# Performance work log

Measured on AMD Instinct MI355X. Metric: run time of the kernel, lower is better.

Reference implementation:

```python
import jax, jax.numpy as jnp
import numpy as np

N = 500_000   # total nodes across the batch of session graphs
B = 8192      # number of graphs
D = 128       # input_dim == output_dim (fc_out is None)
H = 128       # hidden_dim


def setup_inputs() -> dict:
    key = jax.random.key(0)
    ks = jax.random.split(key, 7)
    x_invar = jax.random.normal(ks[0], (N, D), jnp.float32)
    x_var = jax.random.normal(ks[1], (N, D), jnp.float32)
    s = 1.0 / np.sqrt(D)
    Wu = jax.random.normal(ks[2], (H, D), jnp.float32) * s
    bu = jnp.zeros((H,), jnp.float32)
    Wv = jax.random.normal(ks[3], (H, D), jnp.float32) * s
    We = jax.random.normal(ks[4], (1, H), jnp.float32) * (1.0 / np.sqrt(H))
    # sorted segment ids; guarantee every graph has >= 1 node
    seg_ids = jnp.sort(jnp.concatenate([
        jnp.arange(B, dtype=jnp.int32),
        jax.random.randint(ks[5], (N - B,), 0, B, dtype=jnp.int32),
    ]))
    # last node index of each graph = cumsum(counts) - 1
    counts = jax.ops.segment_sum(jnp.ones((N,), jnp.int32), seg_ids, num_segments=B)
    last_nodes = (jnp.cumsum(counts) - 1).astype(jnp.int32)
    return dict(x_invar=x_invar, x_var=x_var, Wu=Wu, bu=bu, Wv=Wv, We=We,
                seg_ids=seg_ids, last_nodes=last_nodes, num_graphs=B)


def _segment_softmax(e, seg, num_segments):
    # e: [M]; numerically stable per-segment softmax
    m = jax.ops.segment_max(e, seg, num_segments=num_segments)
    ex = jnp.exp(e - m[seg])
    den = jax.ops.segment_sum(ex, seg, num_segments=num_segments)
    return ex / den[seg]


def reference(x_invar, x_var, Wu, bu, Wv, We, seg_ids, last_nodes, num_graphs):
    # hybrid granularity, order=1: per-graph [invar; var] node rows.
    # Segment softmax/sum are permutation-invariant within a segment, so we
    # concatenate globally and double the segment ids.
    feats = jnp.concatenate([x_invar, x_var], axis=0)          # [2N, D]
    seg2 = jnp.concatenate([seg_ids, seg_ids], axis=0)         # [2N]
    feat_u = feats @ Wu.T + bu                                 # [2N, H]
    v_invar = (x_invar[last_nodes] @ Wv.T)[seg2]               # [2N, H]
    v_var = (x_var[last_nodes] @ Wv.T)[seg2]                   # [2N, H]
    e_invar = (jax.nn.sigmoid(feat_u + v_invar) @ We.T)[:, 0]  # [2N]
    e_var = (jax.nn.sigmoid(feat_u + v_var) @ We.T)[:, 0]      # [2N]
    a_invar = _segment_softmax(e_invar, seg2, num_graphs)[:, None]
    a_var = _segment_softmax(e_var, seg2, num_graphs)[:, None]
    rst_invar = jax.ops.segment_sum(feats * a_invar, seg2, num_segments=num_graphs)  # [B, D]
    rst_var = jax.ops.segment_sum(feats * a_var, seg2, num_segments=num_graphs)      # [B, D]
    return rst_invar[:, None, :], rst_var[:, None, :]          # [B, 1, D] each (order=1)
```

## Files before the change

kernel.cpp:

```cpp
#include <hip/hip_runtime.h>
#include <stdint.h>

typedef short short8 __attribute__((ext_vector_type(8)));
typedef float f32x4 __attribute__((ext_vector_type(4)));

#define D 128
#define LOG2E 1.44269504088896340736f
#define GPB 4

__device__ __forceinline__ unsigned short f2bf(float f) {
    union { float f; unsigned u; } v; v.f = f;
    unsigned u = v.u;
    unsigned r = (u + 0x7FFFu + ((u >> 16) & 1u)) >> 16;
    return (unsigned short)r;
}

__device__ __forceinline__ unsigned packbf(float x, float y) {
    unsigned ux = __float_as_uint(x) + 0x8000u;
    unsigned uy = __float_as_uint(y) + 0x8000u;
    return __builtin_amdgcn_perm(uy, ux, 0x07060302u);
}

template <int C>
__device__ __forceinline__ float dpp_add(float x) {
    int y = __builtin_amdgcn_update_dpp(0, __float_as_int(x), C, 0xF, 0xF, true);
    return x + __int_as_float(y);
}
__device__ __forceinline__ float red16(float x) {
    x = dpp_add<0xB1>(x);
    x = dpp_add<0x4E>(x);
    x = dpp_add<0x141>(x);
    x = dpp_add<0x140>(x);
    return x;
}

__global__ __launch_bounds__(256) void pack_wu(const float* __restrict__ Wu,
                                               short8* __restrict__ frag) {
    int tid = blockIdx.x * 256 + threadIdx.x;
    int nt = tid >> 8, kk = (tid >> 6) & 3, l = tid & 63;
    int col = nt * 16 + (l & 15);
    int kb  = kk * 32 + ((l >> 4) * 8);
    short8 o;
#pragma unroll
    for (int j = 0; j < 8; ++j) o[j] = (short)f2bf(Wu[col * D + kb + j] * LOG2E);
    frag[tid] = o;
}

__global__ __launch_bounds__(256) void gate_k(const float* __restrict__ xI,
                                              const float* __restrict__ xV,
                                              const float* __restrict__ Wv,
                                              const float* __restrict__ bu,
                                              const int* __restrict__ lastn,
                                              float* __restrict__ cIb,
                                              float* __restrict__ cVb, int B) {
    __shared__ __align__(16) float xs[4][2][D];
    int t = threadIdx.x, h = t & 127, st = t >> 7;
    float bias = bu[h];
    const float4* wv4 = (const float4*)(Wv + (size_t)h * D);
    const float* src = st ? xV : xI;
    float* dst = st ? cVb : cIb;
    int g0 = blockIdx.x * 16;
    for (int p = 0; p < 4; ++p) {
        int gb = g0 + p * 4;
#pragma unroll
        for (int j = 0; j < 4; ++j) {
            int gg = gb + j; if (gg >= B) gg = B - 1;
            xs[j][st][h] = src[(size_t)lastn[gg] * D + h];
        }
        __syncthreads();
        const float4* x0 = (const float4*)xs[0][st];
        const float4* x1 = (const float4*)xs[1][st];
        const float4* x2 = (const float4*)xs[2][st];
        const float4* x3 = (const float4*)xs[3][st];
        float a0 = 0.f, a1 = 0.f, a2 = 0.f, a3 = 0.f;
#pragma unroll
        for (int i = 0; i < 32; ++i) {
            float4 w = wv4[i], b;
            b = x0[i]; a0 += w.x*b.x + w.y*b.y + w.z*b.z + w.w*b.w;
            b = x1[i]; a1 += w.x*b.x + w.y*b.y + w.z*b.z + w.w*b.w;
            b = x2[i]; a2 += w.x*b.x + w.y*b.y + w.z*b.z + w.w*b.w;
            b = x3[i]; a3 += w.x*b.x + w.y*b.y + w.z*b.z + w.w*b.w;
        }
        if (gb + 0 < B) dst[(size_t)(gb+0)*D + h] = __builtin_amdgcn_exp2f(-(a0+bias)*LOG2E);
        if (gb + 1 < B) dst[(size_t)(gb+1)*D + h] = __builtin_amdgcn_exp2f(-(a1+bias)*LOG2E);
        if (gb + 2 < B) dst[(size_t)(gb+2)*D + h] = __builtin_amdgcn_exp2f(-(a2+bias)*LOG2E);
        if (gb + 3 < B) dst[(size_t)(gb+3)*D + h] = __builtin_amdgcn_exp2f(-(a3+bias)*LOG2E);
        __syncthreads();
    }
}

__global__ __launch_bounds__(256) void attn_main(
    const float* __restrict__ xI, const float* __restrict__ xV,
    const float* __restrict__ We, const int* __restrict__ lastn,
    const float* __restrict__ cIb, const float* __restrict__ cVb,
    const short8* __restrict__ fragG, float* __restrict__ out, int B) {
    __shared__ short8 bfrag[2048];
    __shared__ __align__(16) float wt[4][16][2];
    __shared__ float cmbA[2][4][D];
    __shared__ float cmbL[2][4];

    int t = threadIdx.x, lane = t & 63, w = t >> 6;

    {
        const uint4* srcf = (const uint4*)fragG;
        uint4* dst = (uint4*)bfrag;
#pragma unroll
        for (int i = 0; i < 8; ++i) dst[i * 256 + t] = srcf[i * 256 + t];
    }
    float WeR[8];
#pragma unroll
    for (int nt = 0; nt < 8; ++nt) WeR[nt] = We[nt * 16 + (lane & 15)] * LOG2E;
    __syncthreads();

    int g0 = blockIdx.x * GPB;
    int sNext = (g0 == 0) ? 0 : (lastn[g0 - 1] + 1);

    for (int gi = 0; gi < GPB; ++gi) {
        int g = g0 + gi;
        int s = sNext;
        int e = lastn[g] + 1;
        sNext = e;
        int n = e - s;

        float cIr[8], cVr[8];
#pragma unroll
        for (int nt = 0; nt < 8; ++nt) {
            int col = nt * 16 + (lane & 15);
            cIr[nt] = cIb[(size_t)g * D + col];
            cVr[nt] = cVb[(size_t)g * D + col];
        }

        float lIs = 0.f, lVs = 0.f;
        float aI0 = 0.f, aI1 = 0.f, aV0 = 0.f, aV1 = 0.f;

        int ch = (n + 15) >> 4;
        int total = 2 * ch;

        float4 pre[8];
        auto issuePre = [&](int cc) {
            int hf = (cc >= ch) ? 1 : 0;
            const float* sp = (hf ? xV : xI) + ((size_t)s << 7);
            int bb = (cc - hf * ch) << 4;
            int ar = bb + (lane & 15); if (ar > n - 1) ar = n - 1;
            const float* rp = sp + ((size_t)ar << 7) + ((lane >> 4) << 3);
#pragma unroll
            for (int kk = 0; kk < 4; ++kk) {
                pre[2 * kk]     = *(const float4*)(rp + kk * 32);
                pre[2 * kk + 1] = *(const float4*)(rp + kk * 32 + 4);
            }
        };

        if (w < total) issuePre(w);

        for (int c = w; c < total; c += 4) {
            int hf = (c >= ch) ? 1 : 0;
            const float* srcs = (hf ? xV : xI) + ((size_t)s << 7);
            int base = (c - hf * ch) << 4;

            short8 af[4];
#pragma unroll
            for (int kk = 0; kk < 4; ++kk) {
                float4 f0 = pre[2 * kk], f1 = pre[2 * kk + 1];
                union { unsigned u[4]; short8 s8; } cv;
                cv.u[0] = packbf(f0.x, f0.y);
                cv.u[1] = packbf(f0.z, f0.w);
                cv.u[2] = packbf(f1.x, f1.y);
                cv.u[3] = packbf(f1.z, f1.w);
                af[kk] = cv.s8;
            }

            if (c + 4 < total) issuePre(c + 4);

            float pI[4] = {0.f, 0.f, 0.f, 0.f}, pV[4] = {0.f, 0.f, 0.f, 0.f};
#pragma unroll
            for (int nt = 0; nt < 8; ++nt) {
                f32x4 dacc = {0.f, 0.f, 0.f, 0.f};
#pragma unroll
                for (int kk = 0; kk < 4; ++kk)
                    dacc = __builtin_amdgcn_mfma_f32_16x16x32_bf16(
                        af[kk], bfrag[nt * 256 + kk * 64 + lane], dacc, 0, 0, 0);
#pragma unroll
                for (int q = 0; q < 4; ++q) {
                    float t2 = __builtin_amdgcn_exp2f(-dacc[q]);
                    float dI = fmaf(t2, cIr[nt], 1.f);
                    float dV = fmaf(t2, cVr[nt], 1.f);
                    float rr = __builtin_amdgcn_rcpf(dI * dV);
                    pI[q] = fmaf(WeR[nt], dV * rr, pI[q]);
                    pV[q] = fmaf(WeR[nt], dI * rr, pV[q]);
                }
            }

            const float2* s2 = (const float2*)srcs;
            float2 fr[16];
#pragma unroll
            for (int r = 0; r < 16; ++r) {
                int rr = base + r; if (rr > n - 1) rr = n - 1;
                fr[r] = s2[((size_t)rr << 6) + lane];
            }

#pragma unroll
            for (int q = 0; q < 4; ++q) { pI[q] = red16(pI[q]); pV[q] = red16(pV[q]); }
            if (base + 16 > n) {
#pragma unroll
                for (int q = 0; q < 4; ++q) {
                    int r = ((lane >> 4) << 2) + q;
                    if (base + r >= n) { pI[q] = -__builtin_inff(); pV[q] = -__builtin_inff(); }
                }
            }
            float wIq[4], wVq[4];
#pragma unroll
            for (int q = 0; q < 4; ++q) {
                wIq[q] = __builtin_amdgcn_exp2f(pI[q]);
                wVq[q] = __builtin_amdgcn_exp2f(pV[q]);
            }
            lIs += (wIq[0] + wIq[1]) + (wIq[2] + wIq[3]);
            lVs += (wVq[0] + wVq[1]) + (wVq[2] + wVq[3]);

            if ((lane & 15) == 0) {
                int gq = lane >> 4;
                float4 w0 = {wIq[0], wVq[0], wIq[1], wVq[1]};
                float4 w1 = {wIq[2], wVq[2], wIq[3], wVq[3]};
                *(float4*)&wt[w][gq * 4 + 0][0] = w0;
                *(float4*)&wt[w][gq * 4 + 2][0] = w1;
            }

#pragma unroll
            for (int r = 0; r < 16; ++r) {
                float2 f = fr[r];
                float2 wv = *(const float2*)&wt[w][r][0];
                aI0 = fmaf(wv.x, f.x, aI0); aI1 = fmaf(wv.x, f.y, aI1);
                aV0 = fmaf(wv.y, f.x, aV0); aV1 = fmaf(wv.y, f.y, aV1);
            }
        }

        lIs += __shfl_xor(lIs, 16); lIs += __shfl_xor(lIs, 32);
        lVs += __shfl_xor(lVs, 16); lVs += __shfl_xor(lVs, 32);

        __syncthreads();
        {
            float2 vI = {aI0, aI1}, vV = {aV0, aV1};
            *(float2*)&cmbA[0][w][lane * 2] = vI;
            *(float2*)&cmbA[1][w][lane * 2] = vV;
        }
        if (lane == 0) { cmbL[0][w] = lIs; cmbL[1][w] = lVs; }
        __syncthreads();
        {
            int st = t >> 7, d = t & 127;
            float Ls = (cmbL[st][0] + cmbL[st][1]) + (cmbL[st][2] + cmbL[st][3]);
            float A  = (cmbA[st][0][d] + cmbA[st][1][d]) +
                       (cmbA[st][2][d] + cmbA[st][3][d]);
            out[(size_t)st * B * D + (size_t)g * D + d] = A * __builtin_amdgcn_rcpf(Ls);
        }
    }
}

extern "C" void kernel_launch(void* const* d_in, const int* in_sizes, int n_in,
                              void* d_out, int out_size, void* d_ws, size_t ws_size,
                              hipStream_t stream) {
    const float* xI    = (const float*)d_in[0];
    const float* xV    = (const float*)d_in[1];
    const float* Wu    = (const float*)d_in[2];
    const float* bu    = (const float*)d_in[3];
    const float* Wv    = (const float*)d_in[4];
    const float* We    = (const float*)d_in[5];
    const int*   lastn = (const int*)d_in[7];
    const int B = in_sizes[7];

    float*  cIb   = (float*)d_ws;
    float*  cVb   = cIb + (size_t)B * D;
    short8* fragW = (short8*)(cVb + (size_t)B * D);

    pack_wu<<<8, 256, 0, stream>>>(Wu, fragW);
    gate_k<<<(B + 15) / 16, 256, 0, stream>>>(xI, xV, Wv, bu, lastn, cIb, cVb, B);
    attn_main<<<B / GPB, 256, 0, stream>>>(xI, xV, We, lastn, cIb, cVb, fragW,
                                           (float*)d_out, B);
}
```

Baseline: 250.4 us.

## Stage node tiles into LDS via global_load_lds and pack three graph groups per block

Node feature tiles are now loaded once per chunk straight into swizzled LDS buffers using the direct global-to-LDS load. Both the bf16 MFMA A-fragments and the per-row float2 aggregation reads come from that staged copy, so the second global read of the same rows goes away. Blocks grow to 768 threads holding three independent 4-wave groups of two graphs each. The bf16 weight fragments in shared memory are therefore amortised over more waves. In exchange, LDS use rises sharply (about 130KB of staging), which limits occupancy, and full vmcnt/lgkmcnt waits serialise the prefetch.

```diff
diff --git a/kernel.cpp b/kernel.cpp
--- a/kernel.cpp
+++ b/kernel.cpp
@@ -6,7 +6,9 @@
 
 #define D 128
 #define LOG2E 1.44269504088896340736f
-#define GPB 4
+#define NGG  2
+#define NGRP 3
+#define GPBLK (NGG * NGRP)
 
 __device__ __forceinline__ unsigned short f2bf(float f) {
     union { float f; unsigned u; } v; v.f = f;
@@ -32,6 +34,12 @@
     x = dpp_add<0x141>(x);
     x = dpp_add<0x140>(x);
     return x;
+}
+
+__device__ __forceinline__ void gld16(const float* g, float* l) {
+    __builtin_amdgcn_global_load_lds(
+        (const __attribute__((address_space(1))) void*)g,
+        (__attribute__((address_space(3))) void*)l, 16, 0, 0);
 }
 
 __global__ __launch_bounds__(256) void pack_wu(const float* __restrict__ Wu,
@@ -89,78 +97,106 @@
     }
 }
 
-__global__ __launch_bounds__(256) void attn_main(
+__global__ __launch_bounds__(768) void attn_main(
     const float* __restrict__ xI, const float* __restrict__ xV,
     const float* __restrict__ We, const int* __restrict__ lastn,
     const float* __restrict__ cIb, const float* __restrict__ cVb,
     const short8* __restrict__ fragG, float* __restrict__ out, int B) {
     __shared__ short8 bfrag[2048];
-    __shared__ __align__(16) float wt[4][16][2];
-    __shared__ float cmbA[2][4][D];
-    __shared__ float cmbL[2][4];
+    __shared__ __align__(16) float stage[12][2048];
+    __shared__ __align__(16) float wt[12][16][2];
+    __shared__ float cmbA[NGRP][2][4][D];
+    __shared__ float cmbL[NGRP][2][4];
 
     int t = threadIdx.x, lane = t & 63, w = t >> 6;
+    int grp = w >> 2, wiw = w & 3;
 
     {
         const uint4* srcf = (const uint4*)fragG;
         uint4* dst = (uint4*)bfrag;
 #pragma unroll
-        for (int i = 0; i < 8; ++i) dst[i * 256 + t] = srcf[i * 256 + t];
+        for (int i = 0; i < 3; ++i) {
+            int idx = i * 768 + t;
+            if (idx < 2048) dst[idx] = srcf[idx];
+        }
     }
     float WeR[8];
 #pragma unroll
     for (int nt = 0; nt < 8; ++nt) WeR[nt] = We[nt * 16 + (lane & 15)] * LOG2E;
     __syncthreads();
 
-    int g0 = blockIdx.x * GPB;
-    int sNext = (g0 == 0) ? 0 : (lastn[g0 - 1] + 1);
-
-    for (int gi = 0; gi < GPB; ++gi) {
+    float* rb = &stage[w][0];
+    const char* rbc = (const char*)rb;
+
+    int loff[8];
+#pragma unroll
+    for (int i = 0; i < 8; ++i) {
+        int row = (i << 1) + (lane >> 5);
+        loff[i] = (row << 7) + (((lane & 31) ^ (row & 7)) << 2);
+    }
+    int arow = lane & 15;
+    int sw = (arow & 7) << 4;
+    int ab0 = ((arow << 9) + ((lane >> 4) << 5)) ^ sw;
+    int ab1 = ((arow << 9) + ((lane >> 4) << 5) + 16) ^ sw;
+
+    int g0 = blockIdx.x * GPBLK + grp * NGG;
+
+    for (int gi = 0; gi < NGG; ++gi) {
         int g = g0 + gi;
-        int s = sNext;
-        int e = lastn[g] + 1;
-        sNext = e;
-        int n = e - s;
-
+        bool act = (g < B);
+        int s = 0, n = 0, ch = 0, total = 0;
         float cIr[8], cVr[8];
-#pragma unroll
-        for (int nt = 0; nt < 8; ++nt) {
-            int col = nt * 16 + (lane & 15);
-            cIr[nt] = cIb[(size_t)g * D + col];
-            cVr[nt] = cVb[(size_t)g * D + col];
+        if (act) {
+            s = (g == 0) ? 0 : (lastn[g - 1] + 1);
+            n = lastn[g] + 1 - s;
+#pragma unroll
+            for (int nt = 0; nt < 8; ++nt) {
+                int col = nt * 16 + (lane & 15);
+                cIr[nt] = cIb[(size_t)g * D + col];
+                cVr[nt] = cVb[(size_t)g * D + col];
+            }
+            ch = (n + 15) >> 4;
+            total = 2 * ch;
         }
 
         float lIs = 0.f, lVs = 0.f;
         float aI0 = 0.f, aI1 = 0.f, aV0 = 0.f, aV1 = 0.f;
 
-        int ch = (n + 15) >> 4;
-        int total = 2 * ch;
-
-        float4 pre[8];
-        auto issuePre = [&](int cc) {
+        auto issue = [&](int cc) {
             int hf = (cc >= ch) ? 1 : 0;
             const float* sp = (hf ? xV : xI) + ((size_t)s << 7);
             int bb = (cc - hf * ch) << 4;
-            int ar = bb + (lane & 15); if (ar > n - 1) ar = n - 1;
-            const float* rp = sp + ((size_t)ar << 7) + ((lane >> 4) << 3);
+            if (bb + 16 <= n) {
+                const float* pb = sp + ((size_t)bb << 7);
+#pragma unroll
+                for (int i = 0; i < 8; ++i)
+                    gld16(pb + loff[i], rb + (i << 8) + (lane << 2));
+            } else {
+#pragma unroll
+                for (int i = 0; i < 8; ++i) {
+                    int row = (i << 1) + (lane >> 5);
+                    int rr = bb + row; if (rr > n - 1) rr = n - 1;
+                    int lu = (lane & 31) ^ (row & 7);
+                    gld16(sp + ((size_t)rr << 7) + (lu << 2),
+                          rb + (i << 8) + (lane << 2));
+                }
+            }
+        };
+
+        if (wiw < total) issue(wiw);
+
+        for (int c = wiw; c < total; c += 4) {
+            int hf = (c >= ch) ? 1 : 0;
+            int base = (c - hf * ch) << 4;
+
+            asm volatile("s_waitcnt vmcnt(0)" ::: "memory");
+            __builtin_amdgcn_sched_barrier(0);
+
+            short8 af[4];
 #pragma unroll
             for (int kk = 0; kk < 4; ++kk) {
-                pre[2 * kk]     = *(const float4*)(rp + kk * 32);
-                pre[2 * kk + 1] = *(const float4*)(rp + kk * 32 + 4);
-            }
-        };
-
-        if (w < total) issuePre(w);
-
-        for (int c = w; c < total; c += 4) {
-            int hf = (c >= ch) ? 1 : 0;
-            const float* srcs = (hf ? xV : xI) + ((size_t)s << 7);
-            int base = (c - hf * ch) << 4;
-
-            short8 af[4];
-#pragma unroll
-            for (int kk = 0; kk < 4; ++kk) {
-                float4 f0 = pre[2 * kk], f1 = pre[2 * kk + 1];
+                float4 f0 = *(const float4*)(rbc + ab0 + (kk << 7));
+                float4 f1 = *(const float4*)(rbc + ab1 + (kk << 7));
                 union { unsigned u[4]; short8 s8; } cv;
                 cv.u[0] = packbf(f0.x, f0.y);
                 cv.u[1] = packbf(f0.z, f0.w);
@@ -168,8 +204,14 @@
                 cv.u[3] = packbf(f1.z, f1.w);
                 af[kk] = cv.s8;
             }
-
-            if (c + 4 < total) issuePre(c + 4);
+            float2 fr[16];
+#pragma unroll
+            for (int r = 0; r < 16; ++r)
+                fr[r] = *(const float2*)(rbc + ((((r << 9) + (lane << 3)))
+                                               ^ ((r & 7) << 4)));
+            asm volatile("s_waitcnt lgkmcnt(0)" ::: "memory");
+            __builtin_amdgcn_sched_barrier(0);
+            if (c + 4 < total) issue(c + 4);
 
             float pI[4] = {0.f, 0.f, 0.f, 0.f}, pV[4] = {0.f, 0.f, 0.f, 0.f};
 #pragma unroll
@@ -189,15 +231,6 @@
                     pV[q] = fmaf(WeR[nt], dI * rr, pV[q]);
                 }
             }
-
-            const float2* s2 = (const float2*)srcs;
-            float2 fr[16];
-#pragma unroll
-            for (int r = 0; r < 16; ++r) {
-                int rr = base + r; if (rr > n - 1) rr = n - 1;
-                fr[r] = s2[((size_t)rr << 6) + lane];
-            }
-
 #pragma unroll
             for (int q = 0; q < 4; ++q) { pI[q] = red16(pI[q]); pV[q] = red16(pV[q]); }
             if (base + 16 > n) {
@@ -237,18 +270,20 @@
         lVs += __shfl_xor(lVs, 16); lVs += __shfl_xor(lVs, 32);
 
         __syncthreads();
-        {
+        if (act) {
             float2 vI = {aI0, aI1}, vV = {aV0, aV1};
-            *(float2*)&cmbA[0][w][lane * 2] = vI;
-            *(float2*)&cmbA[1][w][lane * 2] = vV;
-        }
-        if (lane == 0) { cmbL[0][w] = lIs; cmbL[1][w] = lVs; }
+            *(float2*)&cmbA[grp][0][wiw][lane * 2] = vI;
+            *(float2*)&cmbA[grp][1][wiw][lane * 2] = vV;
+            if (lane == 0) { cmbL[grp][0][wiw] = lIs; cmbL[grp][1][wiw] = lVs; }
+        }
         __syncthreads();
-        {
-            int st = t >> 7, d = t & 127;
-            float Ls = (cmbL[st][0] + cmbL[st][1]) + (cmbL[st][2] + cmbL[st][3]);
-            float A  = (cmbA[st][0][d] + cmbA[st][1][d]) +
-                       (cmbA[st][2][d] + cmbA[st][3][d]);
+        if (act) {
+            int tig = wiw * 64 + lane;
+            int st = tig >> 7, d = tig & 127;
+            float Ls = (cmbL[grp][st][0] + cmbL[grp][st][1]) +
+                       (cmbL[grp][st][2] + cmbL[grp][st][3]);
+            float A  = (cmbA[grp][st][0][d] + cmbA[grp][st][1][d]) +
+                       (cmbA[grp][st][2][d] + cmbA[grp][st][3][d]);
             out[(size_t)st * B * D + (size_t)g * D + d] = A * __builtin_amdgcn_rcpf(Ls);
         }
     }
@@ -272,6 +307,7 @@
 
     pack_wu<<<8, 256, 0, stream>>>(Wu, fragW);
     gate_k<<<(B + 15) / 16, 256, 0, stream>>>(xI, xV, Wv, bu, lastn, cIb, cVb, B);
-    attn_main<<<B / GPB, 256, 0, stream>>>(xI, xV, We, lastn, cIb, cVb, fragW,
-                                           (float*)d_out, B);
-}
+    int nblk = (B + GPBLK - 1) / GPBLK;
+    attn_main<<<nblk, 768, 0, stream>>>(xI, xV, We, lastn, cIb, cVb, fragW,
+                                        (float*)d_out, B);
+}
```

After: 701.1 us. 180% more time.

## Tile attention over fixed node rows with atomic segment accumulation

Applied to the files above, without the earlier changes.

Replaces the per-graph block loop (4 graphs per block, variable work) with fixed 256-row tiles over the flat node array per stream. Gate values are gathered per row via seg ids, and partial weighted sums and softmax denominators are flushed with global atomics at segment boundaries. A final kernel then normalizes. This targets load imbalance from variable graph sizes, at the cost of atomics, memsets, an extra launch, per-row seg loads, and loss of the register prefetch pipeline. Softmax still has no max subtraction, as before.

```diff
diff --git a/kernel.cpp b/kernel.cpp
--- a/kernel.cpp
+++ b/kernel.cpp
@@ -6,7 +6,6 @@
 
 #define D 128
 #define LOG2E 1.44269504088896340736f
-#define GPB 4
 
 __device__ __forceinline__ unsigned short f2bf(float f) {
     union { float f; unsigned u; } v; v.f = f;
@@ -89,18 +88,18 @@
     }
 }
 
-__global__ __launch_bounds__(256) void attn_main(
+__global__ __launch_bounds__(256) void tile_k(
     const float* __restrict__ xI, const float* __restrict__ xV,
-    const float* __restrict__ We, const int* __restrict__ lastn,
+    const float* __restrict__ We, const int* __restrict__ seg,
     const float* __restrict__ cIb, const float* __restrict__ cVb,
-    const short8* __restrict__ fragG, float* __restrict__ out, int B) {
+    const short8* __restrict__ fragG,
+    float* __restrict__ acc,
+    float* __restrict__ lAcc,
+    int N, int B, int nBS) {
     __shared__ short8 bfrag[2048];
     __shared__ __align__(16) float wt[4][16][2];
-    __shared__ float cmbA[2][4][D];
-    __shared__ float cmbL[2][4];
 
     int t = threadIdx.x, lane = t & 63, w = t >> 6;
-
     {
         const uint4* srcf = (const uint4*)fragG;
         uint4* dst = (uint4*)bfrag;
@@ -112,146 +111,132 @@
     for (int nt = 0; nt < 8; ++nt) WeR[nt] = We[nt * 16 + (lane & 15)] * LOG2E;
     __syncthreads();
 
-    int g0 = blockIdx.x * GPB;
-    int sNext = (g0 == 0) ? 0 : (lastn[g0 - 1] + 1);
-
-    for (int gi = 0; gi < GPB; ++gi) {
-        int g = g0 + gi;
-        int s = sNext;
-        int e = lastn[g] + 1;
-        sNext = e;
-        int n = e - s;
-
-        float cIr[8], cVr[8];
+    int bid = blockIdx.x;
+    int strm = (bid >= nBS) ? 1 : 0;
+    const float* xs = strm ? xV : xI;
+    float* accI = acc;
+    float* accV = acc + (size_t)B * D;
+    int rowBase = (bid - strm * nBS) * 256 + w * 64;
+
+    int curG = -1;
+    float sI0=0.f, sI1=0.f, sV0=0.f, sV1=0.f, lsI=0.f, lsV=0.f;
+
+    for (int rg = 0; rg < 4; ++rg) {
+        int rbase = rowBase + rg * 16;
+        if (rbase >= N) break;
+
+        int arow = rbase + (lane & 15); if (arow > N - 1) arow = N - 1;
+        const float* rp = xs + (size_t)arow * D + ((lane >> 4) << 3);
+        short8 af[4];
+#pragma unroll
+        for (int kk = 0; kk < 4; ++kk) {
+            float4 f0 = *(const float4*)(rp + kk * 32);
+            float4 f1 = *(const float4*)(rp + kk * 32 + 4);
+            union { unsigned u[4]; short8 s8; } cv;
+            cv.u[0] = packbf(f0.x, f0.y);
+            cv.u[1] = packbf(f0.z, f0.w);
+            cv.u[2] = packbf(f1.x, f1.y);
+            cv.u[3] = packbf(f1.z, f1.w);
+            af[kk] = cv.s8;
+        }
+
+        int g4D[4];
+#pragma unroll
+        for (int q = 0; q < 4; ++q) {
+            int r = rbase + ((lane >> 4) << 2) + q; if (r > N - 1) r = N - 1;
+            g4D[q] = seg[r] << 7;
+        }
+
+        float pI[4] = {0.f,0.f,0.f,0.f}, pV[4] = {0.f,0.f,0.f,0.f};
 #pragma unroll
         for (int nt = 0; nt < 8; ++nt) {
             int col = nt * 16 + (lane & 15);
-            cIr[nt] = cIb[(size_t)g * D + col];
-            cVr[nt] = cVb[(size_t)g * D + col];
-        }
-
-        float lIs = 0.f, lVs = 0.f;
-        float aI0 = 0.f, aI1 = 0.f, aV0 = 0.f, aV1 = 0.f;
-
-        int ch = (n + 15) >> 4;
-        int total = 2 * ch;
-
-        float4 pre[8];
-        auto issuePre = [&](int cc) {
-            int hf = (cc >= ch) ? 1 : 0;
-            const float* sp = (hf ? xV : xI) + ((size_t)s << 7);
-            int bb = (cc - hf * ch) << 4;
-            int ar = bb + (lane & 15); if (ar > n - 1) ar = n - 1;
-            const float* rp = sp + ((size_t)ar << 7) + ((lane >> 4) << 3);
-#pragma unroll
-            for (int kk = 0; kk < 4; ++kk) {
-                pre[2 * kk]     = *(const float4*)(rp + kk * 32);
-                pre[2 * kk + 1] = *(const float4*)(rp + kk * 32 + 4);
-            }
-        };
-
-        if (w < total) issuePre(w);
-
-        for (int c = w; c < total; c += 4) {
-            int hf = (c >= ch) ? 1 : 0;
-            const float* srcs = (hf ? xV : xI) + ((size_t)s << 7);
-            int base = (c - hf * ch) << 4;
-
-            short8 af[4];
-#pragma unroll
-            for (int kk = 0; kk < 4; ++kk) {
-                float4 f0 = pre[2 * kk], f1 = pre[2 * kk + 1];
-                union { unsigned u[4]; short8 s8; } cv;
-                cv.u[0] = packbf(f0.x, f0.y);
-                cv.u[1] = packbf(f0.z, f0.w);
-                cv.u[2] = packbf(f1.x, f1.y);
-                cv.u[3] = packbf(f1.z, f1.w);
-                af[kk] = cv.s8;
-            }
-
-            if (c + 4 < total) issuePre(c + 4);
-
-            float pI[4] = {0.f, 0.f, 0.f, 0.f}, pV[4] = {0.f, 0.f, 0.f, 0.f};
-#pragma unroll
-            for (int nt = 0; nt < 8; ++nt) {
-                f32x4 dacc = {0.f, 0.f, 0.f, 0.f};
-#pragma unroll
-                for (int kk = 0; kk < 4; ++kk)
-                    dacc = __builtin_amdgcn_mfma_f32_16x16x32_bf16(
-                        af[kk], bfrag[nt * 256 + kk * 64 + lane], dacc, 0, 0, 0);
-#pragma unroll
-                for (int q = 0; q < 4; ++q) {
-                    float t2 = __builtin_amdgcn_exp2f(-dacc[q]);
-                    float dI = fmaf(t2, cIr[nt], 1.f);
-                    float dV = fmaf(t2, cVr[nt], 1.f);
-                    float rr = __builtin_amdgcn_rcpf(dI * dV);
-                    pI[q] = fmaf(WeR[nt], dV * rr, pI[q]);
-                    pV[q] = fmaf(WeR[nt], dI * rr, pV[q]);
+            float cI4[4], cV4[4];
+#pragma unroll
+            for (int q = 0; q < 4; ++q) {
+                cI4[q] = cIb[g4D[q] + col];
+                cV4[q] = cVb[g4D[q] + col];
+            }
+            f32x4 dacc = {0.f, 0.f, 0.f, 0.f};
+#pragma unroll
+            for (int kk = 0; kk < 4; ++kk)
+                dacc = __builtin_amdgcn_mfma_f32_16x16x32_bf16(
+                    af[kk], bfrag[nt * 256 + kk * 64 + lane], dacc, 0, 0, 0);
+#pragma unroll
+            for (int q = 0; q < 4; ++q) {
+                float t2 = __builtin_amdgcn_exp2f(-dacc[q]);
+                float dI = fmaf(t2, cI4[q], 1.f);
+                float dV = fmaf(t2, cV4[q], 1.f);
+                float rr = __builtin_amdgcn_rcpf(dI * dV);
+                pI[q] = fmaf(WeR[nt], dV * rr, pI[q]);
+                pV[q] = fmaf(WeR[nt], dI * rr, pV[q]);
+            }
+        }
+#pragma unroll
+        for (int q = 0; q < 4; ++q) { pI[q] = red16(pI[q]); pV[q] = red16(pV[q]); }
+        if (rbase + 16 > N) {
+#pragma unroll
+            for (int q = 0; q < 4; ++q) {
+                int r = rbase + ((lane >> 4) << 2) + q;
+                if (r >= N) { pI[q] = -__builtin_inff(); pV[q] = -__builtin_inff(); }
+            }
+        }
+        float wIq[4], wVq[4];
+#pragma unroll
+        for (int q = 0; q < 4; ++q) {
+            wIq[q] = __builtin_amdgcn_exp2f(pI[q]);
+            wVq[q] = __builtin_amdgcn_exp2f(pV[q]);
+        }
+        if ((lane & 15) == 0) {
+            int gq = lane >> 4;
+            float4 w0 = {wIq[0], wVq[0], wIq[1], wVq[1]};
+            float4 w1 = {wIq[2], wVq[2], wIq[3], wVq[3]};
+            *(float4*)&wt[w][gq * 4 + 0][0] = w0;
+            *(float4*)&wt[w][gq * 4 + 2][0] = w1;
+        }
+
+        const float2* s2 = (const float2*)xs;
+        for (int r = 0; r < 16; ++r) {
+            int rr = rbase + r; int rc = rr > N - 1 ? N - 1 : rr;
+            int gr = seg[rc];
+            if (gr != curG) {
+                if (curG >= 0) {
+                    size_t o = ((size_t)curG << 7) + (lane << 1);
+                    atomicAdd(&accI[o], sI0);     atomicAdd(&accI[o + 1], sI1);
+                    atomicAdd(&accV[o], sV0);     atomicAdd(&accV[o + 1], sV1);
+                    if (lane == 0) {
+                        atomicAdd(&lAcc[curG], lsI);
+                        atomicAdd(&lAcc[B + curG], lsV);
+                    }
                 }
-            }
-
-            const float2* s2 = (const float2*)srcs;
-            float2 fr[16];
-#pragma unroll
-            for (int r = 0; r < 16; ++r) {
-                int rr = base + r; if (rr > n - 1) rr = n - 1;
-                fr[r] = s2[((size_t)rr << 6) + lane];
-            }
-
-#pragma unroll
-            for (int q = 0; q < 4; ++q) { pI[q] = red16(pI[q]); pV[q] = red16(pV[q]); }
-            if (base + 16 > n) {
-#pragma unroll
-                for (int q = 0; q < 4; ++q) {
-                    int r = ((lane >> 4) << 2) + q;
-                    if (base + r >= n) { pI[q] = -__builtin_inff(); pV[q] = -__builtin_inff(); }
-                }
-            }
-            float wIq[4], wVq[4];
-#pragma unroll
-            for (int q = 0; q < 4; ++q) {
-                wIq[q] = __builtin_amdgcn_exp2f(pI[q]);
-                wVq[q] = __builtin_amdgcn_exp2f(pV[q]);
-            }
-            lIs += (wIq[0] + wIq[1]) + (wIq[2] + wIq[3]);
-            lVs += (wVq[0] + wVq[1]) + (wVq[2] + wVq[3]);
-
-            if ((lane & 15) == 0) {
-                int gq = lane >> 4;
-                float4 w0 = {wIq[0], wVq[0], wIq[1], wVq[1]};
-                float4 w1 = {wIq[2], wVq[2], wIq[3], wVq[3]};
-                *(float4*)&wt[w][gq * 4 + 0][0] = w0;
-                *(float4*)&wt[w][gq * 4 + 2][0] = w1;
-            }
-
-#pragma unroll
-            for (int r = 0; r < 16; ++r) {
-                float2 f = fr[r];
-                float2 wv = *(const float2*)&wt[w][r][0];
-                aI0 = fmaf(wv.x, f.x, aI0); aI1 = fmaf(wv.x, f.y, aI1);
-                aV0 = fmaf(wv.y, f.x, aV0); aV1 = fmaf(wv.y, f.y, aV1);
-            }
-        }
-
-        lIs += __shfl_xor(lIs, 16); lIs += __shfl_xor(lIs, 32);
-        lVs += __shfl_xor(lVs, 16); lVs += __shfl_xor(lVs, 32);
-
-        __syncthreads();
-        {
-            float2 vI = {aI0, aI1}, vV = {aV0, aV1};
-            *(float2*)&cmbA[0][w][lane * 2] = vI;
-            *(float2*)&cmbA[1][w][lane * 2] = vV;
-        }
-        if (lane == 0) { cmbL[0][w] = lIs; cmbL[1][w] = lVs; }
-        __syncthreads();
-        {
-            int st = t >> 7, d = t & 127;
-            float Ls = (cmbL[st][0] + cmbL[st][1]) + (cmbL[st][2] + cmbL[st][3]);
-            float A  = (cmbA[st][0][d] + cmbA[st][1][d]) +
-                       (cmbA[st][2][d] + cmbA[st][3][d]);
-            out[(size_t)st * B * D + (size_t)g * D + d] = A * __builtin_amdgcn_rcpf(Ls);
-        }
-    }
+                curG = gr; sI0 = sI1 = sV0 = sV1 = lsI = lsV = 0.f;
+            }
+            float2 f = s2[((size_t)rc << 6) + lane];
+            float2 wv = *(const float2*)&wt[w][r][0];
+            sI0 = fmaf(wv.x, f.x, sI0); sI1 = fmaf(wv.x, f.y, sI1);
+            sV0 = fmaf(wv.y, f.x, sV0); sV1 = fmaf(wv.y, f.y, sV1);
+            lsI += wv.x; lsV += wv.y;
+        }
+    }
+    if (curG >= 0) {
+        size_t o = ((size_t)curG << 7) + (lane << 1);
+        atomicAdd(&accI[o], sI0);     atomicAdd(&accI[o + 1], sI1);
+        atomicAdd(&accV[o], sV0);     atomicAdd(&accV[o + 1], sV1);
+        if (lane == 0) {
+            atomicAdd(&lAcc[curG], lsI);
+            atomicAdd(&lAcc[B + curG], lsV);
+        }
+    }
+}
+
+__global__ __launch_bounds__(256) void final_k(float* __restrict__ outp,
+                                               const float* __restrict__ lAcc,
+                                               int B) {
+    int idx = blockIdx.x * 256 + threadIdx.x;
+    int bd = B * D;
+    int st = (idx >= bd) ? 1 : 0;
+    int g = (idx - st * bd) >> 7;
+    outp[idx] = outp[idx] * __builtin_amdgcn_rcpf(lAcc[st * B + g]);
 }
 
 extern "C" void kernel_launch(void* const* d_in, const int* in_sizes, int n_in,
@@ -263,15 +248,23 @@
     const float* bu    = (const float*)d_in[3];
     const float* Wv    = (const float*)d_in[4];
     const float* We    = (const float*)d_in[5];
+    const int*   seg   = (const int*)d_in[6];
     const int*   lastn = (const int*)d_in[7];
     const int B = in_sizes[7];
+    const int N = in_sizes[0] / D;
 
     float*  cIb   = (float*)d_ws;
     float*  cVb   = cIb + (size_t)B * D;
     short8* fragW = (short8*)(cVb + (size_t)B * D);
+    float*  lAcc  = (float*)(fragW + 2048);
+
+    hipMemsetAsync(d_out, 0, (size_t)2 * B * D * sizeof(float), stream);
+    hipMemsetAsync(lAcc, 0, (size_t)2 * B * sizeof(float), stream);
 
     pack_wu<<<8, 256, 0, stream>>>(Wu, fragW);
     gate_k<<<(B + 15) / 16, 256, 0, stream>>>(xI, xV, Wv, bu, lastn, cIb, cVb, B);
-    attn_main<<<B / GPB, 256, 0, stream>>>(xI, xV, We, lastn, cIb, cVb, fragW,
-                                           (float*)d_out, B);
-}
+    int nBS = (N + 255) / 256;
+    tile_k<<<2 * nBS, 256, 0, stream>>>(xI, xV, We, seg, cIb, cVb, fragW,
+                                        (float*)d_out, lAcc, N, B, nBS);
+    final_k<<<(2 * B * D) / 256, 256, 0, stream>>>((float*)d_out, lAcc, B);
+}
```

Measured after the change: 301.4 us. 20.4% more time.

## Launch one block per graph, keep Wu fragments in registers, swap MFMA operands

Applied to the files above, without the earlier changes.

The attention kernel now launches one block per graph instead of four, and drops both the LDS staging of the Wu fragments and the software prefetch of the next chunk. Wu fragments are held in registers (32 short8 per lane), and the MFMA operands are swapped so each lane's accumulator holds hidden units for a single node. That lets the per-node logit be reduced with two cross-lane shuffles instead of DPP row reductions. The aim is more blocks in flight and less LDS traffic, at the cost of higher register pressure, losing the prefetch overlap, and more block launches.

```diff
diff --git a/kernel.cpp b/kernel.cpp
--- a/kernel.cpp
+++ b/kernel.cpp
@@ -6,7 +6,6 @@
 
 #define D 128
 #define LOG2E 1.44269504088896340736f
-#define GPB 4
 
 __device__ __forceinline__ unsigned short f2bf(float f) {
     union { float f; unsigned u; } v; v.f = f;
@@ -19,19 +18,6 @@
     unsigned ux = __float_as_uint(x) + 0x8000u;
     unsigned uy = __float_as_uint(y) + 0x8000u;
     return __builtin_amdgcn_perm(uy, ux, 0x07060302u);
-}
-
-template <int C>
-__device__ __forceinline__ float dpp_add(float x) {
-    int y = __builtin_amdgcn_update_dpp(0, __float_as_int(x), C, 0xF, 0xF, true);
-    return x + __int_as_float(y);
-}
-__device__ __forceinline__ float red16(float x) {
-    x = dpp_add<0xB1>(x);
-    x = dpp_add<0x4E>(x);
-    x = dpp_add<0x141>(x);
-    x = dpp_add<0x140>(x);
-    return x;
 }
 
 __global__ __launch_bounds__(256) void pack_wu(const float* __restrict__ Wu,
@@ -94,163 +80,127 @@
     const float* __restrict__ We, const int* __restrict__ lastn,
     const float* __restrict__ cIb, const float* __restrict__ cVb,
     const short8* __restrict__ fragG, float* __restrict__ out, int B) {
-    __shared__ short8 bfrag[2048];
+    __shared__ __align__(16) float gl[3][D];
     __shared__ __align__(16) float wt[4][16][2];
     __shared__ float cmbA[2][4][D];
     __shared__ float cmbL[2][4];
 
     int t = threadIdx.x, lane = t & 63, w = t >> 6;
+    int g = blockIdx.x;
+
+    short8 wu[8][4];
+#pragma unroll
+    for (int nt = 0; nt < 8; ++nt)
+#pragma unroll
+        for (int kk = 0; kk < 4; ++kk)
+            wu[nt][kk] = fragG[nt * 256 + kk * 64 + lane];
+
+    if (t < D) {
+        gl[0][t] = We[t] * LOG2E;
+        gl[1][t] = cIb[(size_t)g * D + t];
+        gl[2][t] = cVb[(size_t)g * D + t];
+    }
+    __syncthreads();
+
+    int s = (g == 0) ? 0 : (lastn[g - 1] + 1);
+    int n = lastn[g] + 1 - s;
+
+    int ch = (n + 15) >> 4;
+    int total = 2 * ch;
+    int Q4 = (lane >> 4) << 2;
+
+    float lIs = 0.f, lVs = 0.f;
+    float aI0 = 0.f, aI1 = 0.f, aV0 = 0.f, aV1 = 0.f;
+
+    for (int c = w; c < total; c += 4) {
+        int hf = (c >= ch) ? 1 : 0;
+        const float* srcs = (hf ? xV : xI) + ((size_t)s << 7);
+        int base = (c - hf * ch) << 4;
+
+        int arow = base + (lane & 15);
+        bool valid = arow < n;
+        if (arow > n - 1) arow = n - 1;
+        const float* rp = srcs + ((size_t)arow << 7) + ((lane >> 4) << 3);
+        short8 af[4];
+#pragma unroll
+        for (int kk = 0; kk < 4; ++kk) {
+            float4 f0 = *(const float4*)(rp + kk * 32);
+            float4 f1 = *(const float4*)(rp + kk * 32 + 4);
+            union { unsigned u[4]; short8 s8; } cv;
+            cv.u[0] = packbf(f0.x, f0.y);
+            cv.u[1] = packbf(f0.z, f0.w);
+            cv.u[2] = packbf(f1.x, f1.y);
+            cv.u[3] = packbf(f1.z, f1.w);
+            af[kk] = cv.s8;
+        }
+
+        float pI = 0.f, pV = 0.f;
+#pragma unroll
+        for (int nt = 0; nt < 8; ++nt) {
+            f32x4 dacc = {0.f, 0.f, 0.f, 0.f};
+#pragma unroll
+            for (int kk = 0; kk < 4; ++kk)
+                dacc = __builtin_amdgcn_mfma_f32_16x16x32_bf16(
+                    wu[nt][kk], af[kk], dacc, 0, 0, 0);
+            float4 we4 = *(const float4*)&gl[0][nt * 16 + Q4];
+            float4 ci4 = *(const float4*)&gl[1][nt * 16 + Q4];
+            float4 cv4 = *(const float4*)&gl[2][nt * 16 + Q4];
+#pragma unroll
+            for (int q = 0; q < 4; ++q) {
+                float t2 = __builtin_amdgcn_exp2f(-dacc[q]);
+                float dI = fmaf(t2, (&ci4.x)[q], 1.f);
+                float dV = fmaf(t2, (&cv4.x)[q], 1.f);
+                float rr = __builtin_amdgcn_rcpf(dI * dV);
+                pI = fmaf((&we4.x)[q], dV * rr, pI);
+                pV = fmaf((&we4.x)[q], dI * rr, pV);
+            }
+        }
+
+        const float2* s2 = (const float2*)srcs;
+        float2 fr[16];
+#pragma unroll
+        for (int r = 0; r < 16; ++r) {
+            int rr = base + r; if (rr > n - 1) rr = n - 1;
+            fr[r] = s2[((size_t)rr << 6) + lane];
+        }
+
+        pI += __shfl_xor(pI, 16); pI += __shfl_xor(pI, 32);
+        pV += __shfl_xor(pV, 16); pV += __shfl_xor(pV, 32);
+        float wI = valid ? __builtin_amdgcn_exp2f(pI) : 0.f;
+        float wV = valid ? __builtin_amdgcn_exp2f(pV) : 0.f;
+        lIs += wI; lVs += wV;
+
+        if (lane < 16) { float2 wv2 = {wI, wV}; *(float2*)&wt[w][lane][0] = wv2; }
+
+#pragma unroll
+        for (int r = 0; r < 16; ++r) {
+            float2 f = fr[r];
+            float2 wv = *(const float2*)&wt[w][r][0];
+            aI0 = fmaf(wv.x, f.x, aI0); aI1 = fmaf(wv.x, f.y, aI1);
+            aV0 = fmaf(wv.y, f.x, aV0); aV1 = fmaf(wv.y, f.y, aV1);
+        }
+    }
+
+#pragma unroll
+    for (int off = 1; off < 64; off <<= 1) {
+        lIs += __shfl_xor(lIs, off);
+        lVs += __shfl_xor(lVs, off);
+    }
 
     {
-        const uint4* srcf = (const uint4*)fragG;
-        uint4* dst = (uint4*)bfrag;
-#pragma unroll
-        for (int i = 0; i < 8; ++i) dst[i * 256 + t] = srcf[i * 256 + t];
-    }
-    float WeR[8];
-#pragma unroll
-    for (int nt = 0; nt < 8; ++nt) WeR[nt] = We[nt * 16 + (lane & 15)] * LOG2E;
+        float2 vI = {aI0, aI1}, vV = {aV0, aV1};
+        *(float2*)&cmbA[0][w][lane * 2] = vI;
+        *(float2*)&cmbA[1][w][lane * 2] = vV;
+    }
+    if (lane == 0) { cmbL[0][w] = lIs; cmbL[1][w] = lVs; }
     __syncthreads();
-
-    int g0 = blockIdx.x * GPB;
-    int sNext = (g0 == 0) ? 0 : (lastn[g0 - 1] + 1);
-
-    for (int gi = 0; gi < GPB; ++gi) {
-        int g = g0 + gi;
-        int s = sNext;
-        int e = lastn[g] + 1;
-        sNext = e;
-        int n = e - s;
-
-        float cIr[8], cVr[8];
-#pragma unroll
-        for (int nt = 0; nt < 8; ++nt) {
-            int col = nt * 16 + (lane & 15);
-            cIr[nt] = cIb[(size_t)g * D + col];
-            cVr[nt] = cVb[(size_t)g * D + col];
-        }
-
-        float lIs = 0.f, lVs = 0.f;
-        float aI0 = 0.f, aI1 = 0.f, aV0 = 0.f, aV1 = 0.f;
-
-        int ch = (n + 15) >> 4;
-        int total = 2 * ch;
-
-        float4 pre[8];
-        auto issuePre = [&](int cc) {
-            int hf = (cc >= ch) ? 1 : 0;
-            const float* sp = (hf ? xV : xI) + ((size_t)s << 7);
-            int bb = (cc - hf * ch) << 4;
-            int ar = bb + (lane & 15); if (ar > n - 1) ar = n - 1;
-            const float* rp = sp + ((size_t)ar << 7) + ((lane >> 4) << 3);
-#pragma unroll
-            for (int kk = 0; kk < 4; ++kk) {
-                pre[2 * kk]     = *(const float4*)(rp + kk * 32);
-                pre[2 * kk + 1] = *(const float4*)(rp + kk * 32 + 4);
-            }
-        };
-
-        if (w < total) issuePre(w);
-
-        for (int c = w; c < total; c += 4) {
-            int hf = (c >= ch) ? 1 : 0;
-            const float* srcs = (hf ? xV : xI) + ((size_t)s << 7);
-            int base = (c - hf * ch) << 4;
-
-            short8 af[4];
-#pragma unroll
-            for (int kk = 0; kk < 4; ++kk) {
-                float4 f0 = pre[2 * kk], f1 = pre[2 * kk + 1];
-                union { unsigned u[4]; short8 s8; } cv;
-                cv.u[0] = packbf(f0.x, f0.y);
-                cv.u[1] = packbf(f0.z, f0.w);
-                cv.u[2] = packbf(f1.x, f1.y);
-                cv.u[3] = packbf(f1.z, f1.w);
-                af[kk] = cv.s8;
-            }
-
-            if (c + 4 < total) issuePre(c + 4);
-
-            float pI[4] = {0.f, 0.f, 0.f, 0.f}, pV[4] = {0.f, 0.f, 0.f, 0.f};
-#pragma unroll
-            for (int nt = 0; nt < 8; ++nt) {
-                f32x4 dacc = {0.f, 0.f, 0.f, 0.f};
-#pragma unroll
-                for (int kk = 0; kk < 4; ++kk)
-                    dacc = __builtin_amdgcn_mfma_f32_16x16x32_bf16(
-                        af[kk], bfrag[nt * 256 + kk * 64 + lane], dacc, 0, 0, 0);
-#pragma unroll
-                for (int q = 0; q < 4; ++q) {
-                    float t2 = __builtin_amdgcn_exp2f(-dacc[q]);
-                    float dI = fmaf(t2, cIr[nt], 1.f);
-                    float dV = fmaf(t2, cVr[nt], 1.f);
-                    float rr = __builtin_amdgcn_rcpf(dI * dV);
-                    pI[q] = fmaf(WeR[nt], dV * rr, pI[q]);
-                    pV[q] = fmaf(WeR[nt], dI * rr, pV[q]);
-                }
-            }
-
-            const float2* s2 = (const float2*)srcs;
-            float2 fr[16];
-#pragma unroll
-            for (int r = 0; r < 16; ++r) {
-                int rr = base + r; if (rr > n - 1) rr = n - 1;
-                fr[r] = s2[((size_t)rr << 6) + lane];
-            }
-
-#pragma unroll
-            for (int q = 0; q < 4; ++q) { pI[q] = red16(pI[q]); pV[q] = red16(pV[q]); }
-            if (base + 16 > n) {
-#pragma unroll
-                for (int q = 0; q < 4; ++q) {
-                    int r = ((lane >> 4) << 2) + q;
-                    if (base + r >= n) { pI[q] = -__builtin_inff(); pV[q] = -__builtin_inff(); }
-                }
-            }
-            float wIq[4], wVq[4];
-#pragma unroll
-            for (int q = 0; q < 4; ++q) {
-                wIq[q] = __builtin_amdgcn_exp2f(pI[q]);
-                wVq[q] = __builtin_amdgcn_exp2f(pV[q]);
-            }
-            lIs += (wIq[0] + wIq[1]) + (wIq[2] + wIq[3]);
-            lVs += (wVq[0] + wVq[1]) + (wVq[2] + wVq[3]);
-
-            if ((lane & 15) == 0) {
-                int gq = lane >> 4;
-                float4 w0 = {wIq[0], wVq[0], wIq[1], wVq[1]};
-                float4 w1 = {wIq[2], wVq[2], wIq[3], wVq[3]};
-                *(float4*)&wt[w][gq * 4 + 0][0] = w0;
-                *(float4*)&wt[w][gq * 4 + 2][0] = w1;
-            }
-
-#pragma unroll
-            for (int r = 0; r < 16; ++r) {
-                float2 f = fr[r];
-                float2 wv = *(const float2*)&wt[w][r][0];
-                aI0 = fmaf(wv.x, f.x, aI0); aI1 = fmaf(wv.x, f.y, aI1);
-                aV0 = fmaf(wv.y, f.x, aV0); aV1 = fmaf(wv.y, f.y, aV1);
-            }
-        }
-
-        lIs += __shfl_xor(lIs, 16); lIs += __shfl_xor(lIs, 32);
-        lVs += __shfl_xor(lVs, 16); lVs += __shfl_xor(lVs, 32);
-
-        __syncthreads();
-        {
-            float2 vI = {aI0, aI1}, vV = {aV0, aV1};
-            *(float2*)&cmbA[0][w][lane * 2] = vI;
-            *(float2*)&cmbA[1][w][lane * 2] = vV;
-        }
-        if (lane == 0) { cmbL[0][w] = lIs; cmbL[1][w] = lVs; }
-        __syncthreads();
-        {
-            int st = t >> 7, d = t & 127;
-            float Ls = (cmbL[st][0] + cmbL[st][1]) + (cmbL[st][2] + cmbL[st][3]);
-            float A  = (cmbA[st][0][d] + cmbA[st][1][d]) +
-                       (cmbA[st][2][d] + cmbA[st][3][d]);
-            out[(size_t)st * B * D + (size_t)g * D + d] = A * __builtin_amdgcn_rcpf(Ls);
-        }
+    {
+        int st = t >> 7, d = t & 127;
+        float Ls = (cmbL[st][0] + cmbL[st][1]) + (cmbL[st][2] + cmbL[st][3]);
+        float A  = (cmbA[st][0][d] + cmbA[st][1][d]) +
+                   (cmbA[st][2][d] + cmbA[st][3][d]);
+        out[(size_t)st * B * D + (size_t)g * D + d] =
+            A * __builtin_amdgcn_rcpf(Ls * 0.25f);
     }
 }
 
@@ -272,6 +222,6 @@
 
     pack_wu<<<8, 256, 0, stream>>>(Wu, fragW);
     gate_k<<<(B + 15) / 16, 256, 0, stream>>>(xI, xV, Wv, bu, lastn, cIb, cVb, B);
-    attn_main<<<B / GPB, 256, 0, stream>>>(xI, xV, We, lastn, cIb, cVb, fragW,
-                                           (float*)d_out, B);
-}
+    attn_main<<<B, 256, 0, stream>>>(xI, xV, We, lastn, cIb, cVb, fragW,
+                                     (float*)d_out, B);
+}
```

After: 442.9 us. +76.9%, slower.
